# Kernel optimization log

Measured on AMD Instinct MI355X. Metric: run time of the kernel, lower is better.

## Reference

```python
import jax, jax.numpy as jnp
import numpy as np

B, N, FN, FE, OUT = 64, 128, 64, 16, 128
S, VOCAB, EMB, LH = 1033, 1033, 50, 8
MOMO, SIDE, T = 200, 963, 3
LN_EPS, BN_EPS = 1e-12, 1e-5


def setup_inputs():
    key = jax.random.key(0)
    ks = iter(jax.random.split(key, 64))
    def nrm(shape, scale=0.05):
        return jax.random.normal(next(ks), shape, dtype=jnp.float32) * scale
    inp = {}
    inp['adjacency_1'] = (jax.random.uniform(next(ks), (B, N, N)) < 0.1).astype(jnp.float32)
    inp['nodes_1'] = nrm((B, N, FN), 1.0)
    inp['edges_1'] = nrm((B, N, N, FE), 1.0)
    inp['adjacency_2'] = (jax.random.uniform(next(ks), (B, N, N)) < 0.1).astype(jnp.float32)
    inp['nodes_2'] = nrm((B, N, FN), 1.0)
    inp['edges_2'] = nrm((B, N, N, FE), 1.0)
    inp['d1_momo_fts'] = nrm((B, MOMO), 1.0)
    inp['d2_momo_fts'] = nrm((B, MOMO), 1.0)
    inp['d1_protein_fts'] = jax.random.randint(next(ks), (B, S), 0, VOCAB)
    inp['d2_protein_fts'] = jax.random.randint(next(ks), (B, S), 0, VOCAB)
    inp['side_effect'] = nrm((B, SIDE), 1.0)
    inp['word_emb'] = nrm((VOCAB, EMB))
    inp['pos_emb'] = nrm((VOCAB, EMB))
    inp['ln_gamma'] = jnp.ones((EMB,), jnp.float32)
    inp['ln_beta'] = jnp.zeros((EMB,), jnp.float32)
    inp['W_ih'] = nrm((4 * LH, EMB))
    inp['W_hh'] = nrm((4 * LH, LH))
    inp['b_ih'] = jnp.zeros((4 * LH,), jnp.float32)
    inp['b_hh'] = jnp.zeros((4 * LH,), jnp.float32)
    inp['dec_W1'] = nrm((LH * S, 256))
    inp['dec_b1'] = jnp.zeros((256,), jnp.float32)
    inp['bn_gamma'] = jnp.ones((256,), jnp.float32)
    inp['bn_beta'] = jnp.zeros((256,), jnp.float32)
    inp['dec_W2'] = nrm((256, 45))
    inp['dec_b2'] = jnp.zeros((45,), jnp.float32)
    for g in ('1', '2'):
        inp['W_msg' + g] = nrm((FN, FN))
        inp['W_edge' + g] = nrm((FE, FN))
        inp['W_up' + g] = nrm((2 * FN, FN))
        inp['b_up' + g] = jnp.zeros((FN,), jnp.float32)
        inp['W_read' + g] = nrm((2 * FN, OUT))
        inp['b_read' + g] = jnp.zeros((OUT,), jnp.float32)
    inp['W_momo'] = nrm((MOMO, 45))
    inp['b_momo'] = jnp.zeros((45,), jnp.float32)
    inp['W_side'] = nrm((SIDE, 32))
    inp['b_side'] = jnp.zeros((32,), jnp.float32)
    inp['W_final'] = nrm((2 * (OUT + 45 + 45) + 32, 1))
    inp['b_final'] = jnp.zeros((1,), jnp.float32)
    return inp


def _mpnn(adj, nodes, edges, W_msg, W_edge, W_up, b_up, W_read, b_read):
    # Dense-masked equivalent of the padded neighbor/edge gather construction:
    # message[b,n] = sum_m adj[b,n,m] * (h[b,m] @ W_msg + e[b,n,m] @ W_edge)
    node_mask = adj.sum(-1) > 0  # [B,N] -- only connected nodes are updated
    edge_msg = jnp.einsum('bnm,bnmf,fk->bnk', adj, edges, W_edge)  # static over passes
    h = nodes
    for _ in range(T):
        msg = jnp.einsum('bnm,bmf,fk->bnk', adj, h, W_msg) + edge_msg
        upd = jax.nn.relu(jnp.concatenate([h, msg], -1) @ W_up + b_up)
        h = jnp.where(node_mask[..., None], upd, h)
    r = jax.nn.relu(jnp.concatenate([h, nodes], -1) @ W_read + b_read)  # [B,N,OUT]
    return jnp.einsum('bn,bnk->bk', node_mask.astype(h.dtype), r)


def _protein(ids, word_emb, pos_emb, ln_gamma, ln_beta, W_ih, W_hh, b_ih, b_hh,
             dec_W1, dec_b1, bn_gamma, bn_beta, dec_W2, dec_b2):
    x = word_emb[ids] + pos_emb[jnp.arange(S)][None]  # [B,S,EMB]
    u = x.mean(-1, keepdims=True)
    s = ((x - u) ** 2).mean(-1, keepdims=True)
    x = ln_gamma * (x - u) / jnp.sqrt(s + LN_EPS) + ln_beta
    def step(carry, xt):  # torch LSTM gate order: i, f, g, o
        h, c = carry
        gates = xt @ W_ih.T + b_ih + h @ W_hh.T + b_hh
        i, f, g, o = jnp.split(gates, 4, axis=-1)
        c = jax.nn.sigmoid(f) * c + jax.nn.sigmoid(i) * jnp.tanh(g)
        h = jax.nn.sigmoid(o) * jnp.tanh(c)
        return (h, c), h
    h0 = jnp.zeros((ids.shape[0], LH), jnp.float32)
    _, hs = jax.lax.scan(step, (h0, h0), jnp.swapaxes(x, 0, 1))  # [S,B,LH]
    p = jnp.swapaxes(hs, 0, 1).reshape(ids.shape[0], -1)  # [B, S*LH]
    p = jax.nn.relu(p @ dec_W1 + dec_b1)
    m, v = p.mean(0), p.var(0)  # BatchNorm1d in training mode (batch stats)
    p = bn_gamma * (p - m) / jnp.sqrt(v + BN_EPS) + bn_beta
    return p @ dec_W2 + dec_b2  # [B,45]


def reference(adjacency_1, nodes_1, edges_1, adjacency_2, nodes_2, edges_2,
              d1_momo_fts, d1_protein_fts, d2_momo_fts, d2_protein_fts, side_effect,
              word_emb, pos_emb, ln_gamma, ln_beta, W_ih, W_hh, b_ih, b_hh,
              dec_W1, dec_b1, bn_gamma, bn_beta, dec_W2, dec_b2,
              W_msg1, W_edge1, W_up1, b_up1, W_read1, b_read1,
              W_msg2, W_edge2, W_up2, b_up2, W_read2, b_read2,
              W_momo, b_momo, W_side, b_side, W_final, b_final):
    out1 = _mpnn(adjacency_1, nodes_1, edges_1, W_msg1, W_edge1, W_up1, b_up1, W_read1, b_read1)
    out2 = _mpnn(adjacency_2, nodes_2, edges_2, W_msg2, W_edge2, W_up2, b_up2, W_read2, b_read2)
    p1 = _protein(d1_protein_fts, word_emb, pos_emb, ln_gamma, ln_beta, W_ih, W_hh, b_ih, b_hh,
                  dec_W1, dec_b1, bn_gamma, bn_beta, dec_W2, dec_b2)
    p2 = _protein(d2_protein_fts, word_emb, pos_emb, ln_gamma, ln_beta, W_ih, W_hh, b_ih, b_hh,
                  dec_W1, dec_b1, bn_gamma, bn_beta, dec_W2, dec_b2)
    momo1 = d1_momo_fts @ W_momo + b_momo
    momo2 = d2_momo_fts @ W_momo + b_momo
    drug1 = jnp.concatenate([out1, p1, momo1], axis=1)
    drug2 = jnp.concatenate([out2, p2, momo2], axis=1)
    side = side_effect @ W_side + b_side
    feats = jnp.concatenate([drug1, drug2, side], axis=1)
    return feats @ W_final + b_final  # [B,1]
```

## Files before the change

### kernel.cpp

```cpp
#include <hip/hip_runtime.h>
#include <hip/hip_bf16.h>
#include <math.h>

#define Bb 64
#define Nn 128
#define FNf 64
#define Ss 1033
#define EMBe 50

typedef float f4 __attribute__((ext_vector_type(4)));
typedef float f2 __attribute__((ext_vector_type(2)));
typedef int   i4 __attribute__((ext_vector_type(4)));

#define HS_KSTRIDE 1036
#define HS_BSTRIDE 8288
#define HS_PSIZE   530432

constexpr size_t OFF_EMSG  = 2*524288 + 2*524288;
constexpr size_t OFF_MASK  = OFF_EMSG  + 2*524288;
constexpr size_t OFF_OUT12 = OFF_MASK  + 2*8192;
constexpr size_t OFF_PPRE  = OFF_OUT12 + 2*8192;
constexpr size_t OFF_PBN   = OFF_PPRE  + 2*16384;
constexpr size_t OFF_XW    = OFF_PBN   + 2*16384;
constexpr size_t OFF_HS    = OFF_XW    + 2*2115584;
constexpr size_t OFF_W2F   = OFF_HS    + 2*HS_PSIZE;
constexpr size_t OFF_WMF   = OFF_W2F   + 2*256;
constexpr size_t OFF_WSF   = OFF_WMF   + 2*200;
constexpr size_t OFF_CONST = OFF_WSF   + 964;
constexpr size_t OFF_COUNT = OFF_CONST + 4;
constexpr size_t OFF_NZ    = OFF_COUNT + 2*8192;
constexpr size_t OFF_AVAL  = OFF_NZ    + 2*524288;

__device__ inline f4 relu4(f4 v) {
  v[0] = fmaxf(v[0], 0.f); v[1] = fmaxf(v[1], 0.f);
  v[2] = fmaxf(v[2], 0.f); v[3] = fmaxf(v[3], 0.f);
  return v;
}

#define ROR16(x, n) __int_as_float(__builtin_amdgcn_update_dpp(0, __float_as_int(x), 0x120 + (n), 0xF, 0xF, true))

__global__ __launch_bounds__(256) void kA(
    const float* __restrict__ adj1, const float* __restrict__ adj2,
    const float* __restrict__ edges1, const float* __restrict__ edges2,
    const float* __restrict__ We1, const float* __restrict__ We2,
    const int* __restrict__ ids1, const int* __restrict__ ids2,
    const float* __restrict__ we, const float* __restrict__ pe,
    const float* __restrict__ lng, const float* __restrict__ lnb,
    const float* __restrict__ Wih, const float* __restrict__ bih,
    const float* __restrict__ bhh, float* __restrict__ ws) {
  int bid = blockIdx.x;
  int t = threadIdx.x;
  if (bid < 4096) {
    int g = bid >> 11;
    int w = t >> 6, lane = t & 63;
    int row = (bid & 2047) * 4 + w;
    const float* adj   = g ? adj2 : adj1;
    const float* edges = g ? edges2 : edges1;
    const float* We    = g ? We2 : We1;
    float* emsg  = ws + OFF_EMSG + (size_t)g * 524288;
    int*   cntg  = (int*)(ws + OFF_COUNT) + (size_t)g * 8192;
    int*   nz    = (int*)(ws + OFF_NZ)    + (size_t)g * 524288;
    float* aval  = ws + OFF_AVAL + (size_t)g * 524288;

    __shared__ int   lidx[4][64];
    __shared__ float lav[4][64];
    __shared__ float les[4][16];

    const float* arow = adj + (size_t)row * 128;
    float a0 = arow[lane], a1 = arow[64 + lane];
    unsigned long long m0 = __ballot(a0 != 0.f);
    unsigned long long m1 = __ballot(a1 != 0.f);
    int c0 = __popcll(m0);
    int cnt = c0 + __popcll(m1);
    unsigned long long below = ((unsigned long long)1 << lane) - 1ull;
    if (a0 != 0.f) { int pos = __popcll(m0 & below); if (pos < 64) { lidx[w][pos] = lane; lav[w][pos] = a0; } }
    if (a1 != 0.f) { int pos = c0 + __popcll(m1 & below); if (pos < 64) { lidx[w][pos] = lane + 64; lav[w][pos] = a1; } }
    int cc = cnt > 64 ? 64 : cnt;
    __syncthreads();

    nz[(size_t)row * 64 + lane]   = (lane < cc) ? lidx[w][lane] : 0;
    aval[(size_t)row * 64 + lane] = (lane < cc) ? lav[w][lane] : 0.f;

    int f = lane & 15, js = lane >> 4;
    float es = 0.f;
    const float* erow = edges + (size_t)row * 128 * 16;
    for (int j = js; j < cc; j += 4) es += lav[w][j] * erow[lidx[w][j] * 16 + f];
    es += __shfl_xor(es, 16);
    es += __shfl_xor(es, 32);
    if (lane < 16) les[w][lane] = es;
    __syncthreads();

    float acc = 0.f;
    #pragma unroll
    for (int ff = 0; ff < 16; ++ff) acc += les[w][ff] * We[ff * 64 + lane];
    emsg[(size_t)row * 64 + lane] = acc;
    if (lane == 0) cntg[row] = cc;
    return;
  }
  int bid6 = bid - 4096;
  int p = bid6 / 2066;
  int xb = bid6 % 2066;
  const int* ids = p ? ids2 : ids1;
  float* xw = ws + OFF_XW + (size_t)p * 2115584;
  __shared__ float wlds[1600];
  __shared__ float glds[50], blds[50], bs[32];
  __shared__ float xl6[8][52];
  for (int i = t; i < 1600; i += 256) wlds[i] = Wih[i];
  if (t < 50) { glds[t] = lng[t]; blds[t] = lnb[t]; }
  if (t < 32) bs[t] = bih[t] + bhh[t];
  __syncthreads();
  int grp = t >> 5, tl = t & 31;
  int newpos = (tl < 16) ? 2 * tl : 2 * tl - 31;
  const float L = 1.44269504088896f;
  float scale = (tl >= 16 && tl < 24) ? -2.f * L : -L;
  int q0 = xb * 32 + grp * 4;
  for (int qq = 0; qq < 4; ++qq) {
    int q = q0 + qq;
    int s = q % Ss;
    int id = ids[q];
    const float* wr = we + (size_t)id * 50;
    const float* pr = pe + (size_t)s * 50;
    float x1 = wr[tl] + pr[tl];
    bool has2 = (tl + 32) < 50;
    float x2 = has2 ? (wr[tl + 32] + pr[tl + 32]) : 0.f;
    float sm = x1 + x2, sq = x1 * x1 + x2 * x2;
    #pragma unroll
    for (int off = 16; off; off >>= 1) {
      sm += __shfl_xor(sm, off, 32);
      sq += __shfl_xor(sq, off, 32);
    }
    float u = sm * (1.f / 50.f);
    float var = fmaxf(sq * (1.f / 50.f) - u * u, 0.f);
    float rstd = rsqrtf(var + 1e-12f);
    xl6[grp][tl] = glds[tl] * (x1 - u) * rstd + blds[tl];
    if (has2) xl6[grp][tl + 32] = glds[tl + 32] * (x2 - u) * rstd + blds[tl + 32];
    __builtin_amdgcn_wave_barrier();
    float acc = bs[tl];
    #pragma unroll 10
    for (int k = 0; k < 50; ++k) acc += xl6[grp][k] * wlds[tl * 50 + k];
    xw[(size_t)q * 32 + newpos] = acc * scale;
    __builtin_amdgcn_wave_barrier();
  }
}

__global__ __launch_bounds__(256) void kB(
    const float* __restrict__ nodes1, const float* __restrict__ nodes2,
    const float* __restrict__ Wm1, const float* __restrict__ Wm2,
    const float* __restrict__ Wup1, const float* __restrict__ Wup2,
    const float* __restrict__ bup1, const float* __restrict__ bup2,
    const float* __restrict__ Wr1, const float* __restrict__ Wr2,
    const float* __restrict__ br1, const float* __restrict__ br2,
    const float* __restrict__ Whh, float* __restrict__ ws) {
  __shared__ __attribute__((aligned(16))) float hl[8192];
  __shared__ __attribute__((aligned(16))) float xl[8192];
  __shared__ __attribute__((aligned(16))) float wml[4096];
  __shared__ __attribute__((aligned(16))) float wbl[8192];
  int bid = blockIdx.x;
  int t = threadIdx.x;
  if (bid >= 128) {
    if (t >= 64) return;
    int idx = bid - 128;
    int p = idx >> 4, xb = idx & 15;
    const float* xw = ws + OFF_XW + (size_t)p * 2115584;
    float* hs = ws + OFF_HS + (size_t)p * HS_PSIZE;
    int lane16 = t & 15;
    int k = lane16 & 7;
    int half = lane16 >> 3;
    int b = xb * 4 + (t >> 4);
    const float* xwp = xw + (size_t)b * (Ss * 32) + lane16 * 2;
    float* hq = hs + (size_t)b * HS_BSTRIDE + (size_t)k * HS_KSTRIDE;
    const float L = 1.44269504088896f;
    int ga = half ? 8 + k : k;
    int gb = half ? 24 + k : 16 + k;
    float sb_scale = half ? -L : -2.f * L;
    float wa[8], wb[8];
    #pragma unroll
    for (int r = 0; r < 8; ++r) {
      int j = (k - r) & 7;
      wa[r] = -L * Whh[ga * 8 + j];
      wb[r] = sb_scale * Whh[gb * 8 + j];
    }
    float A = half ? 0.f : -4.f * L;
    float B = half ? 1.f : 2.f * L;
    float ho = 0.f, cs = 0.f;
    float q0v = 0.f, q1v = 0.f, q2v = 0.f, q3v = 0.f;

    f2 x[8];
    #pragma unroll
    for (int j = 0; j < 8; ++j) x[j] = *(const f2*)(xwp + (size_t)j * 32);
    const float* pf = xwp + 8 * 32;

    auto step = [&](f2 xc) {
      float h1 = ROR16(ho, 1);
      float h2 = ROR16(ho, 2);
      float h3 = ROR16(ho, 3);
      float h4 = ROR16(ho, 4);
      float h5 = ROR16(ho, 5);
      float h6 = ROR16(ho, 6);
      float h7 = ROR16(ho, 7);
      float a0 = fmaf(ho, wa[0], xc.x);
      float b0 = fmaf(ho, wb[0], xc.y);
      a0 = fmaf(h1, wa[1], a0);  b0 = fmaf(h1, wb[1], b0);
      a0 = fmaf(h2, wa[2], a0);  b0 = fmaf(h2, wb[2], b0);
      a0 = fmaf(h3, wa[3], a0);  b0 = fmaf(h3, wb[3], b0);
      float a1 = h4 * wa[4];     float b1 = h4 * wb[4];
      a1 = fmaf(h5, wa[5], a1);  b1 = fmaf(h5, wb[5], b1);
      a1 = fmaf(h6, wa[6], a1);  b1 = fmaf(h6, wb[6], b1);
      a1 = fmaf(h7, wa[7], a1);  b1 = fmaf(h7, wb[7], b1);
      float acc_a = a0 + a1;
      float acc_b = b0 + b1;
      float ea = __builtin_amdgcn_exp2f(acc_a);
      float sa = __builtin_amdgcn_rcpf(1.f + ea);
      float eb = __builtin_amdgcn_exp2f(acc_b);
      float tb = __builtin_amdgcn_rcpf(1.f + eb);
      float x_own = fmaf(sa * A, tb, sa * B);
      float x_oth = ROR16(x_own, 8);
      float t_oth = ROR16(tb, 8);
      float F  = half ? x_own : x_oth;
      float P2 = half ? x_oth : x_own;
      cs = fmaf(F, cs, P2);
      float e2 = __builtin_amdgcn_exp2f(cs);
      float tc = __builtin_amdgcn_rcpf(1.f + e2);
      float so = half ? tb : t_oth;
      ho = fmaf(so + so, tc, -so);
    };

    for (int g = 0; g < 129; ++g) {
      #pragma unroll
      for (int j = 0; j < 8; ++j) {
        f2 xc = x[j];
        x[j] = *(const f2*)(pf + j * 32);
        step(xc);
        if (j == 0 || j == 4) q0v = ho;
        else if (j == 1 || j == 5) q1v = ho;
        else if (j == 2 || j == 6) q2v = ho;
        else if (j == 3) { q3v = ho; if (!half) *(f4*)(hq + 0) = (f4){q0v, q1v, q2v, q3v}; }
        else { q3v = ho; if (!half) *(f4*)(hq + 4) = (f4){q0v, q1v, q2v, q3v}; }
      }
      pf += 256;
      hq += 8;
    }
    step(x[0]);
    if (!half) hq[0] = ho;
    return;
  }
  int g = bid >> 6, b = bid & 63;
  const float* nodes = g ? nodes2 : nodes1;
  const float* Wm  = g ? Wm2 : Wm1;
  const float* Wup = g ? Wup2 : Wup1;
  const float* bup = g ? bup2 : bup1;
  const float* Wr  = g ? Wr2 : Wr1;
  const float* br  = g ? br2 : br1;
  const float* emsg = ws + OFF_EMSG + (size_t)g * 524288;
  const int*   cntg = (const int*)(ws + OFF_COUNT) + (size_t)g * 8192;
  const int*   nz   = (const int*)(ws + OFF_NZ) + (size_t)g * 524288;
  const float* aval = ws + OFF_AVAL + (size_t)g * 524288;
  float* out12 = ws + OFF_OUT12 + (size_t)g * 8192;

  int col4 = (t & 15) * 4, rg = t >> 4;
  int r0 = rg * 8;
  for (int i = t; i < 4096; i += 256) wml[i] = Wm[i];
  for (int i = t; i < 8192; i += 256) wbl[i] = Wup[i];
  for (int i = t; i < 8192; i += 256) hl[i] = nodes[(size_t)b * 8192 + i];
  __syncthreads();

  for (int it = 0; it < 3; ++it) {
    {
      f4 acc[8];
      #pragma unroll
      for (int rr = 0; rr < 8; ++rr) acc[rr] = (f4){0.f, 0.f, 0.f, 0.f};
      for (int f0 = 0; f0 < 64; f0 += 4) {
        f4 h4[8];
        #pragma unroll
        for (int rr = 0; rr < 8; ++rr) h4[rr] = *(const f4*)&hl[(r0 + rr) * 64 + f0];
        #pragma unroll
        for (int ff = 0; ff < 4; ++ff) {
          f4 w4 = *(const f4*)&wml[(f0 + ff) * 64 + col4];
          #pragma unroll
          for (int rr = 0; rr < 8; ++rr) acc[rr] += h4[rr][ff] * w4;
        }
      }
      #pragma unroll
      for (int rr = 0; rr < 8; ++rr) *(f4*)&xl[(r0 + rr) * 64 + col4] = acc[rr];
    }
    __syncthreads();
    f4 msgv[8];
    #pragma unroll
    for (int rr = 0; rr < 8; ++rr) {
      int row = b * 128 + r0 + rr;
      f4 m = *(const f4*)&emsg[(size_t)row * 64 + col4];
      int cnt4 = (cntg[row] + 3) >> 2;
      const i4* nzr = (const i4*)(nz + (size_t)row * 64);
      const f4* avr = (const f4*)(aval + (size_t)row * 64);
      for (int j4 = 0; j4 < cnt4; ++j4) {
        i4 nq = nzr[j4];
        f4 aq = avr[j4];
        m += aq[0] * *(const f4*)&xl[nq[0] * 64 + col4];
        m += aq[1] * *(const f4*)&xl[nq[1] * 64 + col4];
        m += aq[2] * *(const f4*)&xl[nq[2] * 64 + col4];
        m += aq[3] * *(const f4*)&xl[nq[3] * 64 + col4];
      }
      msgv[rr] = m;
    }
    __syncthreads();
    #pragma unroll
    for (int rr = 0; rr < 8; ++rr) *(f4*)&xl[(r0 + rr) * 64 + col4] = msgv[rr];
    __syncthreads();
    {
      f4 u[8];
      #pragma unroll
      for (int rr = 0; rr < 8; ++rr) u[rr] = *(const f4*)&bup[col4];
      for (int f0 = 0; f0 < 64; f0 += 4) {
        f4 h4[8];
        #pragma unroll
        for (int rr = 0; rr < 8; ++rr) h4[rr] = *(const f4*)&hl[(r0 + rr) * 64 + f0];
        #pragma unroll
        for (int ff = 0; ff < 4; ++ff) {
          f4 w4 = *(const f4*)&wbl[(f0 + ff) * 64 + col4];
          #pragma unroll
          for (int rr = 0; rr < 8; ++rr) u[rr] += h4[rr][ff] * w4;
        }
      }
      for (int f0 = 0; f0 < 64; f0 += 4) {
        f4 m4[8];
        #pragma unroll
        for (int rr = 0; rr < 8; ++rr) m4[rr] = *(const f4*)&xl[(r0 + rr) * 64 + f0];
        #pragma unroll
        for (int ff = 0; ff < 4; ++ff) {
          f4 w4 = *(const f4*)&wbl[(64 + f0 + ff) * 64 + col4];
          #pragma unroll
          for (int rr = 0; rr < 8; ++rr) u[rr] += m4[rr][ff] * w4;
        }
      }
      __syncthreads();
      #pragma unroll
      for (int rr = 0; rr < 8; ++rr) {
        int row = b * 128 + r0 + rr;
        if (cntg[row] > 0) *(f4*)&hl[(r0 + rr) * 64 + col4] = relu4(u[rr]);
      }
    }
    __syncthreads();
  }

  for (int i = t; i < 8192; i += 256) xl[i] = nodes[(size_t)b * 8192 + i];
  __syncthreads();
  for (int kt = 0; kt < 2; ++kt) {
    for (int i = t; i < 8192; i += 256) {
      int f = i >> 6, c = i & 63;
      wbl[i] = Wr[f * 128 + kt * 64 + c];
    }
    __syncthreads();
    f4 part = {0.f, 0.f, 0.f, 0.f};
    {
      f4 u[8];
      #pragma unroll
      for (int rr = 0; rr < 8; ++rr) u[rr] = *(const f4*)&br[kt * 64 + col4];
      for (int f0 = 0; f0 < 64; f0 += 4) {
        f4 h4[8];
        #pragma unroll
        for (int rr = 0; rr < 8; ++rr) h4[rr] = *(const f4*)&hl[(r0 + rr) * 64 + f0];
        #pragma unroll
        for (int ff = 0; ff < 4; ++ff) {
          f4 w4 = *(const f4*)&wbl[(f0 + ff) * 64 + col4];
          #pragma unroll
          for (int rr = 0; rr < 8; ++rr) u[rr] += h4[rr][ff] * w4;
        }
      }
      for (int f0 = 0; f0 < 64; f0 += 4) {
        f4 n4[8];
        #pragma unroll
        for (int rr = 0; rr < 8; ++rr) n4[rr] = *(const f4*)&xl[(r0 + rr) * 64 + f0];
        #pragma unroll
        for (int ff = 0; ff < 4; ++ff) {
          f4 w4 = *(const f4*)&wbl[(64 + f0 + ff) * 64 + col4];
          #pragma unroll
          for (int rr = 0; rr < 8; ++rr) u[rr] += n4[rr][ff] * w4;
        }
      }
      #pragma unroll
      for (int rr = 0; rr < 8; ++rr) {
        int row = b * 128 + r0 + rr;
        if (cntg[row] > 0) part += relu4(u[rr]);
      }
    }
    *(f4*)&wml[rg * 64 + col4] = part;
    __syncthreads();
    for (int off = 8; off; off >>= 1) {
      if (rg < off) {
        f4 v = *(f4*)&wml[rg * 64 + col4] + *(f4*)&wml[(rg + off) * 64 + col4];
        *(f4*)&wml[rg * 64 + col4] = v;
      }
      __syncthreads();
    }
    if (rg == 0) *(f4*)&out12[(size_t)b * 128 + kt * 64 + col4] = *(f4*)&wml[col4];
    __syncthreads();
  }
}

__global__ __launch_bounds__(256) void kC(
    const float* __restrict__ W1,
    const float* __restrict__ W2, const float* __restrict__ b2,
    const float* __restrict__ Wm, const float* __restrict__ bm,
    const float* __restrict__ Wsd, const float* __restrict__ bsd,
    const float* __restrict__ Wf, const float* __restrict__ bf,
    float* __restrict__ ws) {
  int bid = blockIdx.x;
  int t = threadIdx.x;
  if (bid < 256) {
    int ks = bid & 31, jt = (bid >> 5) & 3, p = bid >> 7;
    const float* hs = ws + OFF_HS + (size_t)p * HS_PSIZE;
    float* pp = ws + OFF_PPRE + (size_t)p * 16384;
    int s0 = ks * 32;
    int s1 = (ks == 31) ? Ss : s0 + 32;
    int j0 = jt * 64;
    __shared__ __attribute__((aligned(16))) float hsl[4][768];
    __shared__ __attribute__((aligned(16))) float w1l[4][512];
    int jl = (t & 15) * 4, bb = t >> 4;
    f4 acc[4] = {};
    for (int sb = s0; sb < s1; sb += 4) {
      #pragma unroll
      for (int u = 0; u < 2; ++u) {
        int bk = t + 256 * u;
        int b = bk >> 3, k = bk & 7;
        f4 v = *(const f4*)&hs[(size_t)b * HS_BSTRIDE + (size_t)k * HS_KSTRIDE + sb];
        int c = b * 12 + k;
        hsl[0][c] = v[0]; hsl[1][c] = v[1]; hsl[2][c] = v[2]; hsl[3][c] = v[3];
      }
      #pragma unroll
      for (int u = 0; u < 2; ++u) {
        int idx = t + 256 * u;
        int ss = idx >> 7, l = (idx >> 4) & 7, jj = (idx & 15) * 4;
        int s = sb + ss;
        f4 wv = (s < Ss) ? *(const f4*)&W1[(size_t)(s * 8 + l) * 256 + j0 + jj]
                         : (f4){0.f, 0.f, 0.f, 0.f};
        *(f4*)&w1l[ss][l * 64 + jj] = wv;
      }
      __syncthreads();
      #pragma unroll
      for (int ss = 0; ss < 4; ++ss) {
        f4 r[4][2];
        #pragma unroll
        for (int i = 0; i < 4; ++i) {
          int b = bb + 16 * i;
          r[i][0] = *(const f4*)&hsl[ss][b * 12];
          r[i][1] = *(const f4*)&hsl[ss][b * 12 + 4];
        }
        #pragma unroll
        for (int l = 0; l < 8; ++l) {
          f4 wv = *(const f4*)&w1l[ss][l * 64 + jl];
          #pragma unroll
          for (int i = 0; i < 4; ++i) {
            float hv = (l < 4) ? r[i][0][l] : r[i][1][l - 4];
            acc[i] += hv * wv;
          }
        }
      }
      __syncthreads();
    }
    #pragma unroll
    for (int i = 0; i < 4; ++i) {
      int b = bb + 16 * i;
      float* dst = pp + (size_t)b * 256 + j0 + jl;
      atomicAdd(dst + 0, acc[i][0]); atomicAdd(dst + 1, acc[i][1]);
      atomicAdd(dst + 2, acc[i][2]); atomicAdd(dst + 3, acc[i][3]);
    }
    return;
  }
  __shared__ float wf[468];
  for (int i = t; i < 468; i += 256) wf[i] = Wf[i];
  __syncthreads();
  float* w2f = ws + OFF_W2F;
  float* wmf = ws + OFF_WMF;
  float* wsf = ws + OFF_WSF;
  float* cst = ws + OFF_CONST;
  {
    float a1 = 0.f, a2 = 0.f;
    for (int k = 0; k < 45; ++k) {
      float v = W2[t * 45 + k];
      a1 += v * wf[128 + k];
      a2 += v * wf[346 + k];
    }
    w2f[t] = a1; w2f[256 + t] = a2;
  }
  if (t < 200) {
    float a1 = 0.f, a2 = 0.f;
    for (int k = 0; k < 45; ++k) {
      float v = Wm[t * 45 + k];
      a1 += v * wf[173 + k];
      a2 += v * wf[391 + k];
    }
    wmf[t] = a1; wmf[200 + t] = a2;
  }
  for (int i = t; i < 963; i += 256) {
    float a = 0.f;
    for (int k = 0; k < 32; ++k) a += Wsd[i * 32 + k] * wf[436 + k];
    wsf[i] = a;
  }
  if (t == 0) {
    float cc = bf[0];
    for (int k = 0; k < 45; ++k)
      cc += b2[k] * (wf[128 + k] + wf[346 + k]) + bm[k] * (wf[173 + k] + wf[391 + k]);
    for (int k = 0; k < 32; ++k) cc += bsd[k] * wf[436 + k];
    cst[0] = cc;
  }
}

__global__ __launch_bounds__(256) void kD(
    const float* __restrict__ b1, const float* __restrict__ bng,
    const float* __restrict__ bnb,
    const float* __restrict__ d1m, const float* __restrict__ d2m,
    const float* __restrict__ se, const float* __restrict__ Wf,
    float* __restrict__ ws, float* __restrict__ out) {
  int b = blockIdx.x, t = threadIdx.x;
  const float* out12 = ws + OFF_OUT12;
  const float* pp0 = ws + OFF_PPRE;
  const float* pp1 = ws + OFF_PPRE + 16384;
  const float* w2f = ws + OFF_W2F;
  const float* wmf = ws + OFF_WMF;
  const float* wsf = ws + OFF_WSF;
  float bj = b1[t];
  float sm0 = 0.f, sq0 = 0.f, sm1 = 0.f, sq1 = 0.f;
  for (int bb = 0; bb < 64; ++bb) {
    float v0 = fmaxf(pp0[bb * 256 + t] + bj, 0.f);
    float v1 = fmaxf(pp1[bb * 256 + t] + bj, 0.f);
    sm0 += v0; sq0 += v0 * v0;
    sm1 += v1; sq1 += v1 * v1;
  }
  float m0 = sm0 * (1.f / 64.f);
  float var0 = fmaxf(sq0 * (1.f / 64.f) - m0 * m0, 0.f);
  float rstd0 = rsqrtf(var0 + 1e-5f);
  float sc0 = bng[t] * rstd0, sh0 = bnb[t] - m0 * sc0;
  float m1 = sm1 * (1.f / 64.f);
  float var1 = fmaxf(sq1 * (1.f / 64.f) - m1 * m1, 0.f);
  float rstd1 = rsqrtf(var1 + 1e-5f);
  float sc1 = bng[t] * rstd1, sh1 = bnb[t] - m1 * sc1;
  float val0 = sc0 * fmaxf(pp0[b * 256 + t] + bj, 0.f) + sh0;
  float val1 = sc1 * fmaxf(pp1[b * 256 + t] + bj, 0.f) + sh1;
  float acc = val0 * w2f[t] + val1 * w2f[256 + t];
  if (t < 128) {
    acc += out12[b * 128 + t] * Wf[t];
    acc += out12[8192 + b * 128 + t] * Wf[218 + t];
  }
  if (t < 200) {
    acc += d1m[b * 200 + t] * wmf[t];
    acc += d2m[b * 200 + t] * wmf[200 + t];
  }
  for (int i = t; i < 963; i += 256) acc += se[b * 963 + i] * wsf[i];
  __shared__ float red[256];
  red[t] = acc;
  __syncthreads();
  for (int off = 128; off; off >>= 1) {
    if (t < off) red[t] += red[t + off];
    __syncthreads();
  }
  if (t == 0) out[b] = red[0] + (ws + OFF_CONST)[0];
}

extern "C" void kernel_launch(void* const* d_in, const int* in_sizes, int n_in,
                              void* d_out, int out_size, void* d_ws, size_t ws_size,
                              hipStream_t stream) {
  const float* adj1  = (const float*)d_in[0];
  const float* nodes1= (const float*)d_in[1];
  const float* edges1= (const float*)d_in[2];
  const float* adj2  = (const float*)d_in[3];
  const float* nodes2= (const float*)d_in[4];
  const float* edges2= (const float*)d_in[5];
  const float* d1m   = (const float*)d_in[6];
  const float* d2m   = (const float*)d_in[7];
  const int*   ids1  = (const int*)d_in[8];
  const int*   ids2  = (const int*)d_in[9];
  const float* se    = (const float*)d_in[10];
  const float* we    = (const float*)d_in[11];
  const float* pe    = (const float*)d_in[12];
  const float* lng   = (const float*)d_in[13];
  const float* lnb   = (const float*)d_in[14];
  const float* Wih   = (const float*)d_in[15];
  const float* Whh   = (const float*)d_in[16];
  const float* bih   = (const float*)d_in[17];
  const float* bhh   = (const float*)d_in[18];
  const float* W1    = (const float*)d_in[19];
  const float* b1    = (const float*)d_in[20];
  const float* bng   = (const float*)d_in[21];
  const float* bnb   = (const float*)d_in[22];
  const float* W2    = (const float*)d_in[23];
  const float* b2    = (const float*)d_in[24];
  const float* Wm1   = (const float*)d_in[25];
  const float* We1   = (const float*)d_in[26];
  const float* Wup1  = (const float*)d_in[27];
  const float* bup1  = (const float*)d_in[28];
  const float* Wr1   = (const float*)d_in[29];
  const float* br1   = (const float*)d_in[30];
  const float* Wm2   = (const float*)d_in[31];
  const float* We2   = (const float*)d_in[32];
  const float* Wup2  = (const float*)d_in[33];
  const float* bup2  = (const float*)d_in[34];
  const float* Wr2   = (const float*)d_in[35];
  const float* br2   = (const float*)d_in[36];
  const float* Wmo   = (const float*)d_in[37];
  const float* bmo   = (const float*)d_in[38];
  const float* Wsd   = (const float*)d_in[39];
  const float* bsd   = (const float*)d_in[40];
  const float* Wf    = (const float*)d_in[41];
  const float* bf    = (const float*)d_in[42];
  float* ws = (float*)d_ws;
  float* out = (float*)d_out;

  hipMemsetAsync(ws + OFF_PPRE, 0, 2 * 16384 * sizeof(float), stream);

  kA<<<8228, 256, 0, stream>>>(adj1, adj2, edges1, edges2, We1, We2,
                               ids1, ids2, we, pe, lng, lnb, Wih, bih, bhh, ws);
  kB<<<160, 256, 0, stream>>>(nodes1, nodes2, Wm1, Wm2, Wup1, Wup2, bup1, bup2,
                              Wr1, Wr2, br1, br2, Whh, ws);
  kC<<<257, 256, 0, stream>>>(W1, W2, b2, Wmo, bmo, Wsd, bsd, Wf, bf, ws);
  kD<<<64, 256, 0, stream>>>(b1, bng, bnb, d1m, d2m, se, Wf, ws, out);
}
```

Before: 226.8 us.

## Move adjacency compaction into MPNN blocks and weight folding into embedding kernel

The adjacency compaction and edge-message precompute move out of kA into the per-graph MPNN blocks of kB. Each of those 128 blocks now processes its own 128 rows serially before message passing, and row counts are kept in shared memory. The small final-weight folding block moves from kC to kA, so kC only runs the W1 projection. This shortens kA and lets the edge gather overlap the LSTM recurrence blocks in kB, but it adds serial work to the 128 MPNN blocks, which could lengthen kB's critical path.

```diff
diff --git a/kernel.cpp b/kernel.cpp
--- a/kernel.cpp
+++ b/kernel.cpp
@@ -40,66 +40,60 @@
 #define ROR16(x, n) __int_as_float(__builtin_amdgcn_update_dpp(0, __float_as_int(x), 0x120 + (n), 0xF, 0xF, true))
 
 __global__ __launch_bounds__(256) void kA(
-    const float* __restrict__ adj1, const float* __restrict__ adj2,
-    const float* __restrict__ edges1, const float* __restrict__ edges2,
-    const float* __restrict__ We1, const float* __restrict__ We2,
     const int* __restrict__ ids1, const int* __restrict__ ids2,
     const float* __restrict__ we, const float* __restrict__ pe,
     const float* __restrict__ lng, const float* __restrict__ lnb,
     const float* __restrict__ Wih, const float* __restrict__ bih,
-    const float* __restrict__ bhh, float* __restrict__ ws) {
+    const float* __restrict__ bhh,
+    const float* __restrict__ W2, const float* __restrict__ b2,
+    const float* __restrict__ Wm, const float* __restrict__ bm,
+    const float* __restrict__ Wsd, const float* __restrict__ bsd,
+    const float* __restrict__ Wf, const float* __restrict__ bf,
+    float* __restrict__ ws) {
   int bid = blockIdx.x;
   int t = threadIdx.x;
-  if (bid < 4096) {
-    int g = bid >> 11;
-    int w = t >> 6, lane = t & 63;
-    int row = (bid & 2047) * 4 + w;
-    const float* adj   = g ? adj2 : adj1;
-    const float* edges = g ? edges2 : edges1;
-    const float* We    = g ? We2 : We1;
-    float* emsg  = ws + OFF_EMSG + (size_t)g * 524288;
-    int*   cntg  = (int*)(ws + OFF_COUNT) + (size_t)g * 8192;
-    int*   nz    = (int*)(ws + OFF_NZ)    + (size_t)g * 524288;
-    float* aval  = ws + OFF_AVAL + (size_t)g * 524288;
-
-    __shared__ int   lidx[4][64];
-    __shared__ float lav[4][64];
-    __shared__ float les[4][16];
-
-    const float* arow = adj + (size_t)row * 128;
-    float a0 = arow[lane], a1 = arow[64 + lane];
-    unsigned long long m0 = __ballot(a0 != 0.f);
-    unsigned long long m1 = __ballot(a1 != 0.f);
-    int c0 = __popcll(m0);
-    int cnt = c0 + __popcll(m1);
-    unsigned long long below = ((unsigned long long)1 << lane) - 1ull;
-    if (a0 != 0.f) { int pos = __popcll(m0 & below); if (pos < 64) { lidx[w][pos] = lane; lav[w][pos] = a0; } }
-    if (a1 != 0.f) { int pos = c0 + __popcll(m1 & below); if (pos < 64) { lidx[w][pos] = lane + 64; lav[w][pos] = a1; } }
-    int cc = cnt > 64 ? 64 : cnt;
-    __syncthreads();
-
-    nz[(size_t)row * 64 + lane]   = (lane < cc) ? lidx[w][lane] : 0;
-    aval[(size_t)row * 64 + lane] = (lane < cc) ? lav[w][lane] : 0.f;
-
-    int f = lane & 15, js = lane >> 4;
-    float es = 0.f;
-    const float* erow = edges + (size_t)row * 128 * 16;
-    for (int j = js; j < cc; j += 4) es += lav[w][j] * erow[lidx[w][j] * 16 + f];
-    es += __shfl_xor(es, 16);
-    es += __shfl_xor(es, 32);
-    if (lane < 16) les[w][lane] = es;
-    __syncthreads();
-
-    float acc = 0.f;
-    #pragma unroll
-    for (int ff = 0; ff < 16; ++ff) acc += les[w][ff] * We[ff * 64 + lane];
-    emsg[(size_t)row * 64 + lane] = acc;
-    if (lane == 0) cntg[row] = cc;
+  if (bid >= 4132) {
+    __shared__ float wf[468];
+    for (int i = t; i < 468; i += 256) wf[i] = Wf[i];
+    __syncthreads();
+    float* w2f = ws + OFF_W2F;
+    float* wmf = ws + OFF_WMF;
+    float* wsf = ws + OFF_WSF;
+    float* cst = ws + OFF_CONST;
+    {
+      float a1 = 0.f, a2 = 0.f;
+      for (int k = 0; k < 45; ++k) {
+        float v = W2[t * 45 + k];
+        a1 += v * wf[128 + k];
+        a2 += v * wf[346 + k];
+      }
+      w2f[t] = a1; w2f[256 + t] = a2;
+    }
+    if (t < 200) {
+      float a1 = 0.f, a2 = 0.f;
+      for (int k = 0; k < 45; ++k) {
+        float v = Wm[t * 45 + k];
+        a1 += v * wf[173 + k];
+        a2 += v * wf[391 + k];
+      }
+      wmf[t] = a1; wmf[200 + t] = a2;
+    }
+    for (int i = t; i < 963; i += 256) {
+      float a = 0.f;
+      for (int k = 0; k < 32; ++k) a += Wsd[i * 32 + k] * wf[436 + k];
+      wsf[i] = a;
+    }
+    if (t == 0) {
+      float cc = bf[0];
+      for (int k = 0; k < 45; ++k)
+        cc += b2[k] * (wf[128 + k] + wf[346 + k]) + bm[k] * (wf[173 + k] + wf[391 + k]);
+      for (int k = 0; k < 32; ++k) cc += bsd[k] * wf[436 + k];
+      cst[0] = cc;
+    }
     return;
   }
-  int bid6 = bid - 4096;
-  int p = bid6 / 2066;
-  int xb = bid6 % 2066;
+  int p = bid / 2066;
+  int xb = bid % 2066;
   const int* ids = p ? ids2 : ids1;
   float* xw = ws + OFF_XW + (size_t)p * 2115584;
   __shared__ float wlds[1600];
@@ -145,6 +139,9 @@
 
 __global__ __launch_bounds__(256) void kB(
     const float* __restrict__ nodes1, const float* __restrict__ nodes2,
+    const float* __restrict__ adj1, const float* __restrict__ adj2,
+    const float* __restrict__ edges1, const float* __restrict__ edges2,
+    const float* __restrict__ We1, const float* __restrict__ We2,
     const float* __restrict__ Wm1, const float* __restrict__ Wm2,
     const float* __restrict__ Wup1, const float* __restrict__ Wup2,
     const float* __restrict__ bup1, const float* __restrict__ bup2,
@@ -155,6 +152,7 @@
   __shared__ __attribute__((aligned(16))) float xl[8192];
   __shared__ __attribute__((aligned(16))) float wml[4096];
   __shared__ __attribute__((aligned(16))) float wbl[8192];
+  __shared__ int cnt_l[128];
   int bid = blockIdx.x;
   int t = threadIdx.x;
   if (bid >= 128) {
@@ -246,16 +244,57 @@
   }
   int g = bid >> 6, b = bid & 63;
   const float* nodes = g ? nodes2 : nodes1;
+  const float* adj   = g ? adj2 : adj1;
+  const float* edges = g ? edges2 : edges1;
+  const float* We    = g ? We2 : We1;
   const float* Wm  = g ? Wm2 : Wm1;
   const float* Wup = g ? Wup2 : Wup1;
   const float* bup = g ? bup2 : bup1;
   const float* Wr  = g ? Wr2 : Wr1;
   const float* br  = g ? br2 : br1;
-  const float* emsg = ws + OFF_EMSG + (size_t)g * 524288;
-  const int*   cntg = (const int*)(ws + OFF_COUNT) + (size_t)g * 8192;
-  const int*   nz   = (const int*)(ws + OFF_NZ) + (size_t)g * 524288;
-  const float* aval = ws + OFF_AVAL + (size_t)g * 524288;
+  float* emsg = ws + OFF_EMSG + (size_t)g * 524288;
+  int*   nzg  = (int*)(ws + OFF_NZ) + (size_t)g * 524288;
+  float* aval = ws + OFF_AVAL + (size_t)g * 524288;
   float* out12 = ws + OFF_OUT12 + (size_t)g * 8192;
+
+  {
+    int w = t >> 6, lane = t & 63;
+    int*   lidx = (int*)wml;
+    float* lav  = wml + 256;
+    float* les  = wml + 512;
+    for (int i = 0; i < 32; ++i) {
+      int r = i * 4 + w;
+      size_t row = (size_t)b * 128 + r;
+      const float* arow = adj + row * 128;
+      float a0 = arow[lane], a1 = arow[64 + lane];
+      unsigned long long m0 = __ballot(a0 != 0.f);
+      unsigned long long m1 = __ballot(a1 != 0.f);
+      int c0 = __popcll(m0);
+      int cnt = c0 + __popcll(m1);
+      unsigned long long below = ((unsigned long long)1 << lane) - 1ull;
+      if (a0 != 0.f) { int pos = __popcll(m0 & below); if (pos < 64) { lidx[w * 64 + pos] = lane; lav[w * 64 + pos] = a0; } }
+      if (a1 != 0.f) { int pos = c0 + __popcll(m1 & below); if (pos < 64) { lidx[w * 64 + pos] = lane + 64; lav[w * 64 + pos] = a1; } }
+      int cc = cnt > 64 ? 64 : cnt;
+      __builtin_amdgcn_wave_barrier();
+      nzg[row * 64 + lane]  = (lane < cc) ? lidx[w * 64 + lane] : 0;
+      aval[row * 64 + lane] = (lane < cc) ? lav[w * 64 + lane] : 0.f;
+      int f = lane & 15, js = lane >> 4;
+      float es = 0.f;
+      const float* erow = edges + row * 2048;
+      for (int j = js; j < cc; j += 4) es += lav[w * 64 + j] * erow[lidx[w * 64 + j] * 16 + f];
+      es += __shfl_xor(es, 16);
+      es += __shfl_xor(es, 32);
+      if (lane < 16) les[w * 16 + lane] = es;
+      __builtin_amdgcn_wave_barrier();
+      float eacc = 0.f;
+      #pragma unroll
+      for (int ff = 0; ff < 16; ++ff) eacc += les[w * 16 + ff] * We[ff * 64 + lane];
+      emsg[row * 64 + lane] = eacc;
+      if (lane == 0) cnt_l[r] = cc;
+      __builtin_amdgcn_wave_barrier();
+    }
+  }
+  __syncthreads();
 
   int col4 = (t & 15) * 4, rg = t >> 4;
   int r0 = rg * 8;
@@ -287,11 +326,12 @@
     f4 msgv[8];
     #pragma unroll
     for (int rr = 0; rr < 8; ++rr) {
-      int row = b * 128 + r0 + rr;
-      f4 m = *(const f4*)&emsg[(size_t)row * 64 + col4];
-      int cnt4 = (cntg[row] + 3) >> 2;
-      const i4* nzr = (const i4*)(nz + (size_t)row * 64);
-      const f4* avr = (const f4*)(aval + (size_t)row * 64);
+      int r = r0 + rr;
+      size_t row = (size_t)b * 128 + r;
+      f4 m = *(const f4*)&emsg[row * 64 + col4];
+      int cnt4 = (cnt_l[r] + 3) >> 2;
+      const i4* nzr = (const i4*)(nzg + row * 64);
+      const f4* avr = (const f4*)(aval + row * 64);
       for (int j4 = 0; j4 < cnt4; ++j4) {
         i4 nq = nzr[j4];
         f4 aq = avr[j4];
@@ -335,8 +375,7 @@
       __syncthreads();
       #pragma unroll
       for (int rr = 0; rr < 8; ++rr) {
-        int row = b * 128 + r0 + rr;
-        if (cntg[row] > 0) *(f4*)&hl[(r0 + rr) * 64 + col4] = relu4(u[rr]);
+        if (cnt_l[r0 + rr] > 0) *(f4*)&hl[(r0 + rr) * 64 + col4] = relu4(u[rr]);
       }
     }
     __syncthreads();
@@ -379,8 +418,7 @@
       }
       #pragma unroll
       for (int rr = 0; rr < 8; ++rr) {
-        int row = b * 128 + r0 + rr;
-        if (cntg[row] > 0) part += relu4(u[rr]);
+        if (cnt_l[r0 + rr] > 0) part += relu4(u[rr]);
       }
     }
     *(f4*)&wml[rg * 64 + col4] = part;
@@ -398,110 +436,65 @@
 }
 
 __global__ __launch_bounds__(256) void kC(
-    const float* __restrict__ W1,
-    const float* __restrict__ W2, const float* __restrict__ b2,
-    const float* __restrict__ Wm, const float* __restrict__ bm,
-    const float* __restrict__ Wsd, const float* __restrict__ bsd,
-    const float* __restrict__ Wf, const float* __restrict__ bf,
-    float* __restrict__ ws) {
+    const float* __restrict__ W1, float* __restrict__ ws) {
   int bid = blockIdx.x;
   int t = threadIdx.x;
-  if (bid < 256) {
-    int ks = bid & 31, jt = (bid >> 5) & 3, p = bid >> 7;
-    const float* hs = ws + OFF_HS + (size_t)p * HS_PSIZE;
-    float* pp = ws + OFF_PPRE + (size_t)p * 16384;
-    int s0 = ks * 32;
-    int s1 = (ks == 31) ? Ss : s0 + 32;
-    int j0 = jt * 64;
-    __shared__ __attribute__((aligned(16))) float hsl[4][768];
-    __shared__ __attribute__((aligned(16))) float w1l[4][512];
-    int jl = (t & 15) * 4, bb = t >> 4;
-    f4 acc[4] = {};
-    for (int sb = s0; sb < s1; sb += 4) {
-      #pragma unroll
-      for (int u = 0; u < 2; ++u) {
-        int bk = t + 256 * u;
-        int b = bk >> 3, k = bk & 7;
-        f4 v = *(const f4*)&hs[(size_t)b * HS_BSTRIDE + (size_t)k * HS_KSTRIDE + sb];
-        int c = b * 12 + k;
-        hsl[0][c] = v[0]; hsl[1][c] = v[1]; hsl[2][c] = v[2]; hsl[3][c] = v[3];
-      }
-      #pragma unroll
-      for (int u = 0; u < 2; ++u) {
-        int idx = t + 256 * u;
-        int ss = idx >> 7, l = (idx >> 4) & 7, jj = (idx & 15) * 4;
-        int s = sb + ss;
-        f4 wv = (s < Ss) ? *(const f4*)&W1[(size_t)(s * 8 + l) * 256 + j0 + jj]
-                         : (f4){0.f, 0.f, 0.f, 0.f};
-        *(f4*)&w1l[ss][l * 64 + jj] = wv;
-      }
-      __syncthreads();
-      #pragma unroll
-      for (int ss = 0; ss < 4; ++ss) {
-        f4 r[4][2];
+  int ks = bid & 31, jt = (bid >> 5) & 3, p = bid >> 7;
+  const float* hs = ws + OFF_HS + (size_t)p * HS_PSIZE;
+  float* pp = ws + OFF_PPRE + (size_t)p * 16384;
+  int s0 = ks * 32;
+  int s1 = (ks == 31) ? Ss : s0 + 32;
+  int j0 = jt * 64;
+  __shared__ __attribute__((aligned(16))) float hsl[4][768];
+  __shared__ __attribute__((aligned(16))) float w1l[4][512];
+  int jl = (t & 15) * 4, bb = t >> 4;
+  f4 acc[4] = {};
+  for (int sb = s0; sb < s1; sb += 4) {
+    #pragma unroll
+    for (int u = 0; u < 2; ++u) {
+      int bk = t + 256 * u;
+      int b = bk >> 3, k = bk & 7;
+      f4 v = *(const f4*)&hs[(size_t)b * HS_BSTRIDE + (size_t)k * HS_KSTRIDE + sb];
+      int c = b * 12 + k;
+      hsl[0][c] = v[0]; hsl[1][c] = v[1]; hsl[2][c] = v[2]; hsl[3][c] = v[3];
+    }
+    #pragma unroll
+    for (int u = 0; u < 2; ++u) {
+      int idx = t + 256 * u;
+      int ss = idx >> 7, l = (idx >> 4) & 7, jj = (idx & 15) * 4;
+      int s = sb + ss;
+      f4 wv = (s < Ss) ? *(const f4*)&W1[(size_t)(s * 8 + l) * 256 + j0 + jj]
+                       : (f4){0.f, 0.f, 0.f, 0.f};
+      *(f4*)&w1l[ss][l * 64 + jj] = wv;
+    }
+    __syncthreads();
+    #pragma unroll
+    for (int ss = 0; ss < 4; ++ss) {
+      f4 r[4][2];
+      #pragma unroll
+      for (int i = 0; i < 4; ++i) {
+        int b = bb + 16 * i;
+        r[i][0] = *(const f4*)&hsl[ss][b * 12];
+        r[i][1] = *(const f4*)&hsl[ss][b * 12 + 4];
+      }
+      #pragma unroll
+      for (int l = 0; l < 8; ++l) {
+        f4 wv = *(const f4*)&w1l[ss][l * 64 + jl];
         #pragma unroll
         for (int i = 0; i < 4; ++i) {
-          int b = bb + 16 * i;
-          r[i][0] = *(const f4*)&hsl[ss][b * 12];
-          r[i][1] = *(const f4*)&hsl[ss][b * 12 + 4];
+          float hv = (l < 4) ? r[i][0][l] : r[i][1][l - 4];
+          acc[i] += hv * wv;
         }
-        #pragma unroll
-        for (int l = 0; l < 8; ++l) {
-          f4 wv = *(const f4*)&w1l[ss][l * 64 + jl];
-          #pragma unroll
-          for (int i = 0; i < 4; ++i) {
-            float hv = (l < 4) ? r[i][0][l] : r[i][1][l - 4];
-            acc[i] += hv * wv;
-          }
-        }
-      }
-      __syncthreads();
-    }
-    #pragma unroll
-    for (int i = 0; i < 4; ++i) {
-      int b = bb + 16 * i;
-      float* dst = pp + (size_t)b * 256 + j0 + jl;
-      atomicAdd(dst + 0, acc[i][0]); atomicAdd(dst + 1, acc[i][1]);
-      atomicAdd(dst + 2, acc[i][2]); atomicAdd(dst + 3, acc[i][3]);
-    }
-    return;
-  }
-  __shared__ float wf[468];
-  for (int i = t; i < 468; i += 256) wf[i] = Wf[i];
-  __syncthreads();
-  float* w2f = ws + OFF_W2F;
-  float* wmf = ws + OFF_WMF;
-  float* wsf = ws + OFF_WSF;
-  float* cst = ws + OFF_CONST;
-  {
-    float a1 = 0.f, a2 = 0.f;
-    for (int k = 0; k < 45; ++k) {
-      float v = W2[t * 45 + k];
-      a1 += v * wf[128 + k];
-      a2 += v * wf[346 + k];
-    }
-    w2f[t] = a1; w2f[256 + t] = a2;
-  }
-  if (t < 200) {
-    float a1 = 0.f, a2 = 0.f;
-    for (int k = 0; k < 45; ++k) {
-      float v = Wm[t * 45 + k];
-      a1 += v * wf[173 + k];
-      a2 += v * wf[391 + k];
-    }
-    wmf[t] = a1; wmf[200 + t] = a2;
-  }
-  for (int i = t; i < 963; i += 256) {
-    float a = 0.f;
-    for (int k = 0; k < 32; ++k) a += Wsd[i * 32 + k] * wf[436 + k];
-    wsf[i] = a;
-  }
-  if (t == 0) {
-    float cc = bf[0];
-    for (int k = 0; k < 45; ++k)
-      cc += b2[k] * (wf[128 + k] + wf[346 + k]) + bm[k] * (wf[173 + k] + wf[391 + k]);
-    for (int k = 0; k < 32; ++k) cc += bsd[k] * wf[436 + k];
-    cst[0] = cc;
+      }
+    }
+    __syncthreads();
+  }
+  #pragma unroll
+  for (int i = 0; i < 4; ++i) {
+    int b = bb + 16 * i;
+    float* dst = pp + (size_t)b * 256 + j0 + jl;
+    atomicAdd(dst + 0, acc[i][0]); atomicAdd(dst + 1, acc[i][1]);
+    atomicAdd(dst + 2, acc[i][2]); atomicAdd(dst + 3, acc[i][3]);
   }
 }
 
@@ -607,10 +600,11 @@
 
   hipMemsetAsync(ws + OFF_PPRE, 0, 2 * 16384 * sizeof(float), stream);
 
-  kA<<<8228, 256, 0, stream>>>(adj1, adj2, edges1, edges2, We1, We2,
-                               ids1, ids2, we, pe, lng, lnb, Wih, bih, bhh, ws);
-  kB<<<160, 256, 0, stream>>>(nodes1, nodes2, Wm1, Wm2, Wup1, Wup2, bup1, bup2,
+  kA<<<4133, 256, 0, stream>>>(ids1, ids2, we, pe, lng, lnb, Wih, bih, bhh,
+                               W2, b2, Wmo, bmo, Wsd, bsd, Wf, bf, ws);
+  kB<<<160, 256, 0, stream>>>(nodes1, nodes2, adj1, adj2, edges1, edges2,
+                              We1, We2, Wm1, Wm2, Wup1, Wup2, bup1, bup2,
                               Wr1, Wr2, br1, br2, Whh, ws);
-  kC<<<257, 256, 0, stream>>>(W1, W2, b2, Wmo, bmo, Wsd, bsd, Wf, bf, ws);
+  kC<<<256, 256, 0, stream>>>(W1, ws);
   kD<<<64, 256, 0, stream>>>(b1, bng, bnb, d1m, d2m, se, Wf, ws, out);
 }
```

Result: slower. 243.4 us (+7.3%).
